# Kernel tuning notes

Measured on AMD Instinct MI355X. Metric: run time of the kernel, lower is better.

The kernel has to match this reference:

```python
import jax, jax.numpy as jnp
import numpy as np

DROPOUT = 0.2  # dropout radius in normalized [0,1] coords
EPS = 1e-08


def setup_inputs() -> dict:
    key = jax.random.key(0)
    k1, k2, k3, k4 = jax.random.split(key, 4)
    B, C, T = 64, 273, 3000
    brain_sig = jax.random.normal(k1, (B, C, T), dtype=jnp.float32)
    positions = jax.random.uniform(k2, (B, C, 2), dtype=jnp.float32)
    center = jax.random.uniform(k3, (2,), dtype=jnp.float32)
    mc_centers = jax.random.uniform(k4, (100, 2), dtype=jnp.float32)
    return {"brain_sig": brain_sig, "positions": positions,
            "center": center, "mc_centers": mc_centers}


def reference(brain_sig, positions, center, mc_centers):
    # kept channels: distance from ban center > dropout radius  -> (B, C)
    kept = jnp.linalg.norm(positions - center, axis=-1) > DROPOUT
    out = brain_sig * kept[:, :, None].astype(brain_sig.dtype)
    # Monte-Carlo estimate of keep probability (100 trials, vectorized)
    # diffs: (N, B, C, 2)
    diffs = positions[None, :, :, :] - mc_centers[:, None, None, :]
    kept_mc = jnp.linalg.norm(diffs, axis=-1) > DROPOUT  # (N, B, C)
    proba_kept = jnp.mean(kept_mc.astype(brain_sig.dtype), axis=0)  # (B, C)
    out = out / (EPS + proba_kept[:, :, None])
    return out
```

## Files before the change

### kernel.cpp

```cpp
#include <hip/hip_runtime.h>
#include <math.h>


__global__ __launch_bounds__(256) void channel_dropout_kernel(
    const float* __restrict__ sig,
    const float* __restrict__ pos,
    const float* __restrict__ center,
    const float* __restrict__ mc,
    float* __restrict__ out,
    int T, int NMC)
{
    const int row = blockIdx.x;
    const int t   = threadIdx.x;
    __shared__ float s_scale;

    if (t < 64) {
        const float px = pos[2 * row + 0];
        const float py = pos[2 * row + 1];
        float cnt = 0.0f;
        for (int i = t; i < NMC; i += 64) {
            const float dx = px - mc[2 * i + 0];
            const float dy = py - mc[2 * i + 1];
            cnt += (sqrtf(dx * dx + dy * dy) > 0.2f) ? 1.0f : 0.0f;
        }
        #pragma unroll
        for (int off = 32; off > 0; off >>= 1)
            cnt += __shfl_down(cnt, off, 64);
        if (t == 0) {
            const float dx = px - center[0];
            const float dy = py - center[1];
            const float kept =
                (sqrtf(dx * dx + dy * dy) > 0.2f) ? 1.0f : 0.0f;
            const float proba = cnt / (float)NMC;
            s_scale = kept / (1e-8f + proba);
        }
    }
    __syncthreads();
    const float scale = s_scale;

    const size_t base = (size_t)row * (size_t)T;
    const int n4 = T >> 2;
    const float4* __restrict__ in4  = (const float4*)(sig + base);
    float4* __restrict__       out4 = (float4*)(out + base);

    for (int i = t; i < n4; i += 256) {
        float4 v = in4[i];
        v.x *= scale; v.y *= scale; v.z *= scale; v.w *= scale;
        out4[i] = v;
    }
    for (int i = (n4 << 2) + t; i < T; i += 256) {
        out[base + i] = sig[base + i] * scale;
    }
}

extern "C" void kernel_launch(void* const* d_in, const int* in_sizes, int n_in,
                              void* d_out, int out_size, void* d_ws, size_t ws_size,
                              hipStream_t stream) {
    const float* sig    = (const float*)d_in[0];
    const float* pos    = (const float*)d_in[1];
    const float* center = (const float*)d_in[2];
    const float* mc     = (const float*)d_in[3];
    float* out          = (float*)d_out;

    const int rows = in_sizes[1] / 2;
    const int T    = in_sizes[0] / rows;
    const int NMC  = in_sizes[3] / 2;

    channel_dropout_kernel<<<rows, 256, 0, stream>>>(
        sig, pos, center, mc, out, T, NMC);
}
```

Measured before the change: 349.5 us.

## Overlap signal loads with per-wave MC scale compute, use nontemporal accesses

The row's signal loads (up to four float4 per thread) are issued before the dropout scale is computed, so memory latency overlaps the Monte-Carlo distance loop. Every wave now computes the scale redundantly with an xor-shuffle reduction, which removes the shared-memory broadcast and the __syncthreads barrier. Loads and stores use nontemporal builtins to avoid polluting the cache on this streaming workload. The cost is redundant ALU work in each wave and more registers held for the prefetched values.

```diff
diff --git a/kernel.cpp b/kernel.cpp
--- a/kernel.cpp
+++ b/kernel.cpp
@@ -1,6 +1,8 @@
 #include <hip/hip_runtime.h>
 #include <math.h>
 
+
+typedef float v4f __attribute__((ext_vector_type(4)));
 
 __global__ __launch_bounds__(256) void channel_dropout_kernel(
     const float* __restrict__ sig,
@@ -10,43 +12,55 @@
     float* __restrict__ out,
     int T, int NMC)
 {
-    const int row = blockIdx.x;
-    const int t   = threadIdx.x;
-    __shared__ float s_scale;
-
-    if (t < 64) {
-        const float px = pos[2 * row + 0];
-        const float py = pos[2 * row + 1];
-        float cnt = 0.0f;
-        for (int i = t; i < NMC; i += 64) {
-            const float dx = px - mc[2 * i + 0];
-            const float dy = py - mc[2 * i + 1];
-            cnt += (sqrtf(dx * dx + dy * dy) > 0.2f) ? 1.0f : 0.0f;
-        }
-        #pragma unroll
-        for (int off = 32; off > 0; off >>= 1)
-            cnt += __shfl_down(cnt, off, 64);
-        if (t == 0) {
-            const float dx = px - center[0];
-            const float dy = py - center[1];
-            const float kept =
-                (sqrtf(dx * dx + dy * dy) > 0.2f) ? 1.0f : 0.0f;
-            const float proba = cnt / (float)NMC;
-            s_scale = kept / (1e-8f + proba);
-        }
-    }
-    __syncthreads();
-    const float scale = s_scale;
+    const int row  = blockIdx.x;
+    const int t    = threadIdx.x;
+    const int lane = t & 63;
 
     const size_t base = (size_t)row * (size_t)T;
     const int n4 = T >> 2;
-    const float4* __restrict__ in4  = (const float4*)(sig + base);
-    float4* __restrict__       out4 = (float4*)(out + base);
+    const v4f* __restrict__ in4  = (const v4f*)(sig + base);
+    v4f* __restrict__       out4 = (v4f*)(out + base);
 
-    for (int i = t; i < n4; i += 256) {
-        float4 v = in4[i];
-        v.x *= scale; v.y *= scale; v.z *= scale; v.w *= scale;
-        out4[i] = v;
+    v4f v[4];
+    #pragma unroll
+    for (int u = 0; u < 4; ++u) {
+        const int i = t + u * 256;
+        if (i < n4) v[u] = __builtin_nontemporal_load(in4 + i);
+    }
+
+    const float px = pos[2 * row + 0];
+    const float py = pos[2 * row + 1];
+    const float cx = center[0];
+    const float cy = center[1];
+
+    float cnt = 0.0f;
+    for (int i = lane; i < NMC; i += 64) {
+        const float dx = px - mc[2 * i + 0];
+        const float dy = py - mc[2 * i + 1];
+        cnt += (sqrtf(dx * dx + dy * dy) > 0.2f) ? 1.0f : 0.0f;
+    }
+    #pragma unroll
+    for (int off = 32; off > 0; off >>= 1)
+        cnt += __shfl_xor(cnt, off, 64);
+
+    const float ddx  = px - cx;
+    const float ddy  = py - cy;
+    const float kept = (sqrtf(ddx * ddx + ddy * ddy) > 0.2f) ? 1.0f : 0.0f;
+    const float scale = kept / (1e-8f + cnt / (float)NMC);
+
+    #pragma unroll
+    for (int u = 0; u < 4; ++u) {
+        const int i = t + u * 256;
+        if (i < n4) {
+            v4f r = v[u];
+            r *= scale;
+            __builtin_nontemporal_store(r, out4 + i);
+        }
+    }
+    for (int i = t + 1024; i < n4; i += 256) {
+        v4f r = __builtin_nontemporal_load(in4 + i);
+        r *= scale;
+        __builtin_nontemporal_store(r, out4 + i);
     }
     for (int i = (n4 << 2) + t; i < T; i += 256) {
         out[base + i] = sig[base + i] * scale;
```

Measured after the change: 341.1 us. -2.4%, faster.
